# Performance work log

Hardware: AMD Instinct MI355X
Metric: run time of the kernel (lower is better)

Reference implementation:

```python
import jax, jax.numpy as jnp
import numpy as np
import math

B, S, D, H = 4, 1024, 1024, 16
DK = D // H
WINDOW = 128
NEG = -100000.0


def setup_inputs() -> dict:
    key = jax.random.key(0)
    kx, kw1, kb1, kw2, kb2 = jax.random.split(key, 5)
    x = jax.random.normal(kx, (B, S, D), dtype=jnp.float32)
    # sliding-window band mask: True where |i-j| <= WINDOW
    i = jnp.arange(S)
    band = (jnp.abs(i[:, None] - i[None, :]) <= WINDOW)
    mask = jnp.broadcast_to(band, (B, S, S))
    # second structured mask: causal
    causal = (i[:, None] >= i[None, :])
    mask2 = jnp.broadcast_to(causal, (B, S, S))
    scale = 1.0 / math.sqrt(D)
    Wqkv = jax.random.normal(kw1, (D, 3 * D), dtype=jnp.float32) * scale
    bqkv = jax.random.normal(kb1, (3 * D,), dtype=jnp.float32) * 0.01
    Wo = jax.random.normal(kw2, (D, D), dtype=jnp.float32) * scale
    bo = jax.random.normal(kb2, (D,), dtype=jnp.float32) * 0.01
    return {"x": x, "mask": mask, "mask2": mask2, "Wqkv": Wqkv, "bqkv": bqkv, "Wo": Wo, "bo": bo}


def reference(x, mask, mask2, Wqkv, bqkv, Wo, bo):
    b, s, d = x.shape
    qkv = x @ Wqkv + bqkv                      # [b, s, 3d]
    q, k, v = jnp.split(qkv, 3, axis=-1)
    # [b, s, h, dk] -> [b, h, s, dk]
    q = q.reshape(b, s, H, DK).transpose(0, 2, 1, 3)
    k = k.reshape(b, s, H, DK).transpose(0, 2, 1, 3)
    v = v.reshape(b, s, H, DK).transpose(0, 2, 1, 3)
    scores = jnp.einsum('bhtd,bhsd->bhts', q, k) / math.sqrt(DK)
    scores = jnp.where(mask[:, None, :, :], scores, NEG)
    scores = jnp.where(mask2[:, None, :, :], scores, NEG)
    weights = jax.nn.softmax(scores, axis=-1)  # [b, h, t, s]
    context = jnp.einsum('bhts,bhsd->bhtd', weights, v)
    context = context.transpose(0, 2, 1, 3).reshape(b, s, d)
    context = context @ Wo + bo
    return (context, weights)
```

## Files before the change

### kernel.cpp

```cpp
#include <hip/hip_runtime.h>

typedef short bf16x8 __attribute__((ext_vector_type(8)));
typedef float floatx4 __attribute__((ext_vector_type(4)));

#define GLOBAL_AS __attribute__((address_space(1)))
#define LDS_AS __attribute__((address_space(3)))

__device__ __forceinline__ void gload_lds16(const ushort* g, ushort* l) {
  __builtin_amdgcn_global_load_lds((const GLOBAL_AS void*)g, (LDS_AS void*)l, 16, 0, 0);
}

__device__ __forceinline__ ushort f2bf(float x) {
  uint u = __float_as_uint(x);
  return (ushort)((u + 0x7fffu + ((u >> 16) & 1u)) >> 16);
}

__global__ __launch_bounds__(256) void k_f32_to_bf16(const float4* __restrict__ in,
                                                     ushort4* __restrict__ out, int n4) {
  int g = blockIdx.x * 256 + threadIdx.x;
  if (g < n4) {
    float4 v = in[g];
    ushort4 o;
    o.x = f2bf(v.x); o.y = f2bf(v.y); o.z = f2bf(v.z); o.w = f2bf(v.w);
    out[g] = o;
  }
}

__global__ __launch_bounds__(256) void k_transpose2(const float* __restrict__ W1,
                                                    ushort* __restrict__ O1,
                                                    const float* __restrict__ W2,
                                                    ushort* __restrict__ O2) {
  __shared__ float tile[32][33];
  int bx = blockIdx.x;
  const float* in; ushort* out; int N;
  if (bx < 96) { in = W1; out = O1; N = 3072; }
  else         { in = W2; out = O2; N = 1024; bx -= 96; }
  const int K = 1024;
  int n0 = bx * 32, k0 = blockIdx.y * 32;
  int tx = threadIdx.x & 31, ty = threadIdx.x >> 5;
  #pragma unroll
  for (int r = ty; r < 32; r += 8)
    tile[r][tx] = in[(size_t)(k0 + r) * N + n0 + tx];
  __syncthreads();
  #pragma unroll
  for (int r = ty; r < 32; r += 8)
    out[(size_t)(n0 + r) * K + k0 + tx] = f2bf(tile[tx][r]);
}

template <int OUT_BF16, int BN>
__global__ __launch_bounds__(256) void k_gemm_bt(const ushort* __restrict__ A,
                                                 const ushort* __restrict__ Bt,
                                                 const float* __restrict__ bias,
                                                 void* __restrict__ Cout,
                                                 int M, int N, int K) {
  constexpr int NI = BN / 32;
  constexpr int NB = BN / 64;
  __shared__ ushort As[128 * 32];
  __shared__ ushort Bs[BN * 32];
  const int t = threadIdx.x;
  const int m0 = blockIdx.y * 128, n0 = blockIdx.x * BN;
  const int w = t >> 6, l = t & 63;
  const int wm = (w & 1) * 64, wn = (w >> 1) * (BN / 2);
  const int lr = l & 15, q8 = (l >> 4) * 8;
  const int lrow = l >> 2, lcol = (l & 3) * 8;

  floatx4 acc[4][NI];
  #pragma unroll
  for (int i = 0; i < 4; ++i)
    #pragma unroll
    for (int j = 0; j < NI; ++j) acc[i][j] = (floatx4){0.f, 0.f, 0.f, 0.f};

  for (int k0 = 0; k0 < K; k0 += 32) {
    __syncthreads();
    #pragma unroll
    for (int i = 0; i < 2; ++i) {
      int r0 = (w * 2 + i) * 16;
      gload_lds16(A + (size_t)(m0 + r0 + lrow) * K + k0 + lcol, As + r0 * 32);
    }
    #pragma unroll
    for (int i = 0; i < NB; ++i) {
      int r0 = (w * NB + i) * 16;
      gload_lds16(Bt + (size_t)(n0 + r0 + lrow) * K + k0 + lcol, Bs + r0 * 32);
    }
    __syncthreads();
    bf16x8 af[4], bfr[NI];
    #pragma unroll
    for (int mi = 0; mi < 4; ++mi)
      af[mi] = *(const bf16x8*)(As + (wm + mi * 16 + lr) * 32 + q8);
    #pragma unroll
    for (int ni = 0; ni < NI; ++ni)
      bfr[ni] = *(const bf16x8*)(Bs + (wn + ni * 16 + lr) * 32 + q8);
    #pragma unroll
    for (int mi = 0; mi < 4; ++mi)
      #pragma unroll
      for (int ni = 0; ni < NI; ++ni)
        acc[mi][ni] = __builtin_amdgcn_mfma_f32_16x16x32_bf16(af[mi], bfr[ni], acc[mi][ni], 0, 0, 0);
  }

  const int rq = (l >> 4) * 4;
  #pragma unroll
  for (int ni = 0; ni < NI; ++ni) {
    int col = n0 + wn + ni * 16 + lr;
    float bv = bias[col];
    #pragma unroll
    for (int mi = 0; mi < 4; ++mi) {
      int row = m0 + wm + mi * 16 + rq;
      #pragma unroll
      for (int r2 = 0; r2 < 4; ++r2) {
        float v = acc[mi][ni][r2] + bv;
        size_t idx = (size_t)(row + r2) * N + col;
        if (OUT_BF16) ((ushort*)Cout)[idx] = f2bf(v);
        else          ((float*)Cout)[idx] = v;
      }
    }
  }
}

__global__ __launch_bounds__(256) void k_attn(const ushort* __restrict__ qkv,
                                              float* __restrict__ wout,
                                              ushort* __restrict__ ctxout) {
  __shared__ float smA[64][68];
  __shared__ float smB[64 * 68];
  __shared__ float smInv[64];

  const int t = threadIdx.x;
  const int tj = t & 15, ti = t >> 4;
  const int iblk = blockIdx.x & 15;
  const int h = (blockIdx.x >> 4) & 15;
  const int b = blockIdx.x >> 8;
  const int i0 = iblk * 64;
  const int tok0 = b * 1024 + i0;
  const int qoff = h * 64, koff = 1024 + h * 64, voff = 2048 + h * 64;
  const size_t wbase = ((size_t)(b * 16 + h) * 1024 + i0) * 1024;

  {
    int jstart = i0 - 128; if (jstart < 0) jstart = 0;
    int jend = i0 + 64;
    float4 z = {0.f, 0.f, 0.f, 0.f};
    for (int g = t; g < 64 * 256; g += 256) {
      int r = g >> 8, j = (g & 255) * 4;
      if (j < jstart || j >= jend)
        *(float4*)(wout + wbase + (size_t)r * 1024 + j) = z;
    }
  }

  for (int cc = t; cc < 512; cc += 256) {
    int r = cc >> 3, c8 = (cc & 7) * 8;
    uint4 u = *(const uint4*)(qkv + (size_t)(tok0 + r) * 3072 + qoff + c8);
    float4 f0, f1;
    f0.x = __uint_as_float(u.x << 16); f0.y = __uint_as_float(u.x & 0xffff0000u);
    f0.z = __uint_as_float(u.y << 16); f0.w = __uint_as_float(u.y & 0xffff0000u);
    f1.x = __uint_as_float(u.z << 16); f1.y = __uint_as_float(u.z & 0xffff0000u);
    f1.z = __uint_as_float(u.w << 16); f1.w = __uint_as_float(u.w & 0xffff0000u);
    *(float4*)&smA[r][c8] = f0;
    *(float4*)&smA[r][c8 + 4] = f1;
  }

  float sreg[3][4][4];
  float mrun[4], lrun[4];
  #pragma unroll
  for (int ri = 0; ri < 4; ++ri) { mrun[ri] = -3e38f; lrun[ri] = 0.f; }

  #pragma unroll
  for (int bb = 0; bb < 3; ++bb) {
    const int jb = i0 - 128 + bb * 64;
    if (jb < 0) continue;
    __syncthreads();
    for (int cc = t; cc < 512; cc += 256) {
      int r = cc >> 3, c8 = (cc & 7) * 8;
      uint4 u = *(const uint4*)(qkv + (size_t)(b * 1024 + jb + r) * 3072 + koff + c8);
      float4 f0, f1;
      f0.x = __uint_as_float(u.x << 16); f0.y = __uint_as_float(u.x & 0xffff0000u);
      f0.z = __uint_as_float(u.y << 16); f0.w = __uint_as_float(u.y & 0xffff0000u);
      f1.x = __uint_as_float(u.z << 16); f1.y = __uint_as_float(u.z & 0xffff0000u);
      f1.z = __uint_as_float(u.w << 16); f1.w = __uint_as_float(u.w & 0xffff0000u);
      *(float4*)&smB[r * 68 + c8] = f0;
      *(float4*)&smB[r * 68 + c8 + 4] = f1;
    }
    __syncthreads();

    float sacc[4][4];
    #pragma unroll
    for (int ri = 0; ri < 4; ++ri)
      #pragma unroll
      for (int ci = 0; ci < 4; ++ci) sacc[ri][ci] = 0.f;

    for (int d4 = 0; d4 < 16; ++d4) {
      float4 qv[4], kv[4];
      #pragma unroll
      for (int ri = 0; ri < 4; ++ri) qv[ri] = *(const float4*)&smA[4 * ti + ri][d4 * 4];
      #pragma unroll
      for (int ci = 0; ci < 4; ++ci) kv[ci] = *(const float4*)&smB[(tj + 16 * ci) * 68 + d4 * 4];
      #pragma unroll
      for (int ri = 0; ri < 4; ++ri)
        #pragma unroll
        for (int ci = 0; ci < 4; ++ci)
          sacc[ri][ci] += qv[ri].x * kv[ci].x + qv[ri].y * kv[ci].y +
                          qv[ri].z * kv[ci].z + qv[ri].w * kv[ci].w;
    }

    #pragma unroll
    for (int ri = 0; ri < 4; ++ri) {
      int gi = i0 + 4 * ti + ri;
      float mx = mrun[ri];
      #pragma unroll
      for (int ci = 0; ci < 4; ++ci) {
        int gj = jb + tj + 16 * ci;
        bool valid = (gj <= gi) && (gi - gj <= 128);
        float s = valid ? sacc[ri][ci] * 0.125f : -3e38f;
        sreg[bb][ri][ci] = s;
        mx = fmaxf(mx, s);
      }
      float sum = lrun[ri] * __expf(mrun[ri] - mx);
      #pragma unroll
      for (int ci = 0; ci < 4; ++ci) {
        float s = sreg[bb][ri][ci];
        sum += (s > -1e37f) ? __expf(s - mx) : 0.f;
      }
      mrun[ri] = mx; lrun[ri] = sum;
    }
  }

  float mfin[4], minv[4];
  #pragma unroll
  for (int ri = 0; ri < 4; ++ri) {
    float m = mrun[ri], lsum = lrun[ri];
    #pragma unroll
    for (int off = 1; off < 16; off <<= 1) {
      float mo = __shfl_xor(m, off, 64);
      float lo = __shfl_xor(lsum, off, 64);
      float mn = fmaxf(m, mo);
      lsum = lsum * __expf(m - mn) + lo * __expf(mo - mn);
      m = mn;
    }
    mfin[ri] = m;
    minv[ri] = 1.0f / lsum;
  }
  if (tj == 0) {
    #pragma unroll
    for (int ri = 0; ri < 4; ++ri) smInv[4 * ti + ri] = minv[ri];
  }

  float ctx[4][4];
  #pragma unroll
  for (int ri = 0; ri < 4; ++ri)
    #pragma unroll
    for (int ci = 0; ci < 4; ++ci) ctx[ri][ci] = 0.f;

  #pragma unroll
  for (int bb = 0; bb < 3; ++bb) {
    const int jb = i0 - 128 + bb * 64;
    if (jb < 0) continue;
    __syncthreads();
    for (int cc = t; cc < 512; cc += 256) {
      int r = cc >> 3, c8 = (cc & 7) * 8;
      uint4 u = *(const uint4*)(qkv + (size_t)(b * 1024 + jb + r) * 3072 + voff + c8);
      float* bT = smB + r;
      bT[(c8 + 0) * 67] = __uint_as_float(u.x << 16);
      bT[(c8 + 1) * 67] = __uint_as_float(u.x & 0xffff0000u);
      bT[(c8 + 2) * 67] = __uint_as_float(u.y << 16);
      bT[(c8 + 3) * 67] = __uint_as_float(u.y & 0xffff0000u);
      bT[(c8 + 4) * 67] = __uint_as_float(u.z << 16);
      bT[(c8 + 5) * 67] = __uint_as_float(u.z & 0xffff0000u);
      bT[(c8 + 6) * 67] = __uint_as_float(u.w << 16);
      bT[(c8 + 7) * 67] = __uint_as_float(u.w & 0xffff0000u);
    }
    #pragma unroll
    for (int ri = 0; ri < 4; ++ri) {
      int r = 4 * ti + ri;
      float mr = mfin[ri];
      #pragma unroll
      for (int ci = 0; ci < 4; ++ci) {
        float s = sreg[bb][ri][ci];
        smA[r][tj + 16 * ci] = (s > -1e37f) ? __expf(s - mr) : 0.f;
      }
    }
    __syncthreads();
    for (int g = t; g < 1024; g += 256) {
      int r = g >> 4, c = (g & 15) * 4;
      float4 e4 = *(const float4*)&smA[r][c];
      float iv = smInv[r];
      float4 o = {e4.x * iv, e4.y * iv, e4.z * iv, e4.w * iv};
      *(float4*)(wout + wbase + (size_t)r * 1024 + jb + c) = o;
    }
    #pragma unroll 4
    for (int jl4 = 0; jl4 < 64; jl4 += 4) {
      float4 wv4[4], vv4[4];
      #pragma unroll
      for (int ri = 0; ri < 4; ++ri) wv4[ri] = *(const float4*)&smA[4 * ti + ri][jl4];
      #pragma unroll
      for (int ci = 0; ci < 4; ++ci) vv4[ci] = *(const float4*)(smB + (tj + 16 * ci) * 67 + jl4);
      #pragma unroll
      for (int ri = 0; ri < 4; ++ri)
        #pragma unroll
        for (int ci = 0; ci < 4; ++ci)
          ctx[ri][ci] += wv4[ri].x * vv4[ci].x + wv4[ri].y * vv4[ci].y +
                         wv4[ri].z * vv4[ci].z + wv4[ri].w * vv4[ci].w;
    }
  }

  #pragma unroll
  for (int ri = 0; ri < 4; ++ri) {
    int r = 4 * ti + ri;
    float iv = minv[ri];
    #pragma unroll
    for (int ci = 0; ci < 4; ++ci)
      ctxout[(size_t)(tok0 + r) * 1024 + qoff + tj + 16 * ci] = f2bf(ctx[ri][ci] * iv);
  }
}

extern "C" void kernel_launch(void* const* d_in, const int* in_sizes, int n_in,
                              void* d_out, int out_size, void* d_ws, size_t ws_size,
                              hipStream_t stream) {
  const float* x    = (const float*)d_in[0];
  const float* Wqkv = (const float*)d_in[3];
  const float* bqkv = (const float*)d_in[4];
  const float* Wo   = (const float*)d_in[5];
  const float* bo   = (const float*)d_in[6];

  float* out_ctx = (float*)d_out;
  float* out_w   = out_ctx + (size_t)4 * 1024 * 1024;

  char* ws = (char*)d_ws;
  ushort* qkv_bf = (ushort*)(ws);
  ushort* ctx_bf = (ushort*)(ws + 25165824);
  ushort* x_bf   = (ushort*)(ws + 33554432);
  ushort* WqkvT  = (ushort*)(ws + 41943040);
  ushort* WoT    = (ushort*)(ws + 48234496);

  k_f32_to_bf16<<<4096, 256, 0, stream>>>((const float4*)x, (ushort4*)x_bf, 1048576);
  k_transpose2<<<dim3(128, 32), 256, 0, stream>>>(Wqkv, WqkvT, Wo, WoT);
  k_gemm_bt<1, 128><<<dim3(24, 32), 256, 0, stream>>>(x_bf, WqkvT, bqkv, qkv_bf, 4096, 3072, 1024);
  k_attn<<<1024, 256, 0, stream>>>(qkv_bf, out_w, ctx_bf);
  k_gemm_bt<0, 64><<<dim3(16, 32), 256, 0, stream>>>(ctx_bf, WoT, bo, out_ctx, 4096, 1024, 1024);
}
```

Baseline: 443.6 us.

## Rewrite windowed attention kernel with bf16 MFMA and single-pass softmax

Replaces the scalar fp32 FMA attention kernel with one that uses bf16 MFMA 16x16x32 instructions for both QK^T and PV. All 192 K and V rows of the window are loaded into LDS at once, kept as bf16 (V stored transposed), so the three-block online softmax becomes a single pass with one max and one sum reduction. This removes the per-block syncs and the fp32 conversion work. In exchange it uses more LDS per block, writes the weights output as scattered scalar stores, and feeds bf16-rounded probabilities into PV.

```diff
diff --git a/kernel.cpp b/kernel.cpp
--- a/kernel.cpp
+++ b/kernel.cpp
@@ -119,22 +119,24 @@
 __global__ __launch_bounds__(256) void k_attn(const ushort* __restrict__ qkv,
                                               float* __restrict__ wout,
                                               ushort* __restrict__ ctxout) {
-  __shared__ float smA[64][68];
-  __shared__ float smB[64 * 68];
-  __shared__ float smInv[64];
+  __shared__ ushort smKP[192 * 68];
+  __shared__ ushort smVT[64 * 202];
+  __shared__ ushort smQ[64 * 68];
 
   const int t = threadIdx.x;
-  const int tj = t & 15, ti = t >> 4;
+  const int w = t >> 6, l = t & 63;
+  const int lr = l & 15, q8 = (l >> 4) * 8, q4 = (l >> 4) * 4;
   const int iblk = blockIdx.x & 15;
   const int h = (blockIdx.x >> 4) & 15;
   const int b = blockIdx.x >> 8;
   const int i0 = iblk * 64;
+  const int jb0 = i0 - 128;
   const int tok0 = b * 1024 + i0;
   const int qoff = h * 64, koff = 1024 + h * 64, voff = 2048 + h * 64;
   const size_t wbase = ((size_t)(b * 16 + h) * 1024 + i0) * 1024;
 
   {
-    int jstart = i0 - 128; if (jstart < 0) jstart = 0;
+    int jstart = jb0 < 0 ? 0 : jb0;
     int jend = i0 + 64;
     float4 z = {0.f, 0.f, 0.f, 0.f};
     for (int g = t; g < 64 * 256; g += 256) {
@@ -144,168 +146,125 @@
     }
   }
 
-  for (int cc = t; cc < 512; cc += 256) {
-    int r = cc >> 3, c8 = (cc & 7) * 8;
-    uint4 u = *(const uint4*)(qkv + (size_t)(tok0 + r) * 3072 + qoff + c8);
-    float4 f0, f1;
-    f0.x = __uint_as_float(u.x << 16); f0.y = __uint_as_float(u.x & 0xffff0000u);
-    f0.z = __uint_as_float(u.y << 16); f0.w = __uint_as_float(u.y & 0xffff0000u);
-    f1.x = __uint_as_float(u.z << 16); f1.y = __uint_as_float(u.z & 0xffff0000u);
-    f1.z = __uint_as_float(u.w << 16); f1.w = __uint_as_float(u.w & 0xffff0000u);
-    *(float4*)&smA[r][c8] = f0;
-    *(float4*)&smA[r][c8 + 4] = f1;
-  }
-
-  float sreg[3][4][4];
-  float mrun[4], lrun[4];
-  #pragma unroll
-  for (int ri = 0; ri < 4; ++ri) { mrun[ri] = -3e38f; lrun[ri] = 0.f; }
-
-  #pragma unroll
-  for (int bb = 0; bb < 3; ++bb) {
-    const int jb = i0 - 128 + bb * 64;
-    if (jb < 0) continue;
-    __syncthreads();
-    for (int cc = t; cc < 512; cc += 256) {
-      int r = cc >> 3, c8 = (cc & 7) * 8;
-      uint4 u = *(const uint4*)(qkv + (size_t)(b * 1024 + jb + r) * 3072 + koff + c8);
-      float4 f0, f1;
-      f0.x = __uint_as_float(u.x << 16); f0.y = __uint_as_float(u.x & 0xffff0000u);
-      f0.z = __uint_as_float(u.y << 16); f0.w = __uint_as_float(u.y & 0xffff0000u);
-      f1.x = __uint_as_float(u.z << 16); f1.y = __uint_as_float(u.z & 0xffff0000u);
-      f1.z = __uint_as_float(u.w << 16); f1.w = __uint_as_float(u.w & 0xffff0000u);
-      *(float4*)&smB[r * 68 + c8] = f0;
-      *(float4*)&smB[r * 68 + c8 + 4] = f1;
-    }
-    __syncthreads();
-
-    float sacc[4][4];
-    #pragma unroll
-    for (int ri = 0; ri < 4; ++ri)
-      #pragma unroll
-      for (int ci = 0; ci < 4; ++ci) sacc[ri][ci] = 0.f;
-
-    for (int d4 = 0; d4 < 16; ++d4) {
-      float4 qv[4], kv[4];
-      #pragma unroll
-      for (int ri = 0; ri < 4; ++ri) qv[ri] = *(const float4*)&smA[4 * ti + ri][d4 * 4];
-      #pragma unroll
-      for (int ci = 0; ci < 4; ++ci) kv[ci] = *(const float4*)&smB[(tj + 16 * ci) * 68 + d4 * 4];
-      #pragma unroll
-      for (int ri = 0; ri < 4; ++ri)
-        #pragma unroll
-        for (int ci = 0; ci < 4; ++ci)
-          sacc[ri][ci] += qv[ri].x * kv[ci].x + qv[ri].y * kv[ci].y +
-                          qv[ri].z * kv[ci].z + qv[ri].w * kv[ci].w;
-    }
-
-    #pragma unroll
-    for (int ri = 0; ri < 4; ++ri) {
-      int gi = i0 + 4 * ti + ri;
-      float mx = mrun[ri];
-      #pragma unroll
-      for (int ci = 0; ci < 4; ++ci) {
-        int gj = jb + tj + 16 * ci;
-        bool valid = (gj <= gi) && (gi - gj <= 128);
-        float s = valid ? sacc[ri][ci] * 0.125f : -3e38f;
-        sreg[bb][ri][ci] = s;
-        mx = fmaxf(mx, s);
-      }
-      float sum = lrun[ri] * __expf(mrun[ri] - mx);
-      #pragma unroll
-      for (int ci = 0; ci < 4; ++ci) {
-        float s = sreg[bb][ri][ci];
-        sum += (s > -1e37f) ? __expf(s - mx) : 0.f;
-      }
-      mrun[ri] = mx; lrun[ri] = sum;
-    }
-  }
-
-  float mfin[4], minv[4];
-  #pragma unroll
-  for (int ri = 0; ri < 4; ++ri) {
-    float m = mrun[ri], lsum = lrun[ri];
-    #pragma unroll
-    for (int off = 1; off < 16; off <<= 1) {
-      float mo = __shfl_xor(m, off, 64);
-      float lo = __shfl_xor(lsum, off, 64);
-      float mn = fmaxf(m, mo);
-      lsum = lsum * __expf(m - mn) + lo * __expf(mo - mn);
-      m = mn;
-    }
-    mfin[ri] = m;
-    minv[ri] = 1.0f / lsum;
-  }
-  if (tj == 0) {
-    #pragma unroll
-    for (int ri = 0; ri < 4; ++ri) smInv[4 * ti + ri] = minv[ri];
-  }
-
-  float ctx[4][4];
-  #pragma unroll
-  for (int ri = 0; ri < 4; ++ri)
-    #pragma unroll
-    for (int ci = 0; ci < 4; ++ci) ctx[ri][ci] = 0.f;
-
-  #pragma unroll
-  for (int bb = 0; bb < 3; ++bb) {
-    const int jb = i0 - 128 + bb * 64;
-    if (jb < 0) continue;
-    __syncthreads();
-    for (int cc = t; cc < 512; cc += 256) {
-      int r = cc >> 3, c8 = (cc & 7) * 8;
-      uint4 u = *(const uint4*)(qkv + (size_t)(b * 1024 + jb + r) * 3072 + voff + c8);
-      float* bT = smB + r;
-      bT[(c8 + 0) * 67] = __uint_as_float(u.x << 16);
-      bT[(c8 + 1) * 67] = __uint_as_float(u.x & 0xffff0000u);
-      bT[(c8 + 2) * 67] = __uint_as_float(u.y << 16);
-      bT[(c8 + 3) * 67] = __uint_as_float(u.y & 0xffff0000u);
-      bT[(c8 + 4) * 67] = __uint_as_float(u.z << 16);
-      bT[(c8 + 5) * 67] = __uint_as_float(u.z & 0xffff0000u);
-      bT[(c8 + 6) * 67] = __uint_as_float(u.w << 16);
-      bT[(c8 + 7) * 67] = __uint_as_float(u.w & 0xffff0000u);
-    }
-    #pragma unroll
-    for (int ri = 0; ri < 4; ++ri) {
-      int r = 4 * ti + ri;
-      float mr = mfin[ri];
-      #pragma unroll
-      for (int ci = 0; ci < 4; ++ci) {
-        float s = sreg[bb][ri][ci];
-        smA[r][tj + 16 * ci] = (s > -1e37f) ? __expf(s - mr) : 0.f;
-      }
-    }
-    __syncthreads();
-    for (int g = t; g < 1024; g += 256) {
-      int r = g >> 4, c = (g & 15) * 4;
-      float4 e4 = *(const float4*)&smA[r][c];
-      float iv = smInv[r];
-      float4 o = {e4.x * iv, e4.y * iv, e4.z * iv, e4.w * iv};
-      *(float4*)(wout + wbase + (size_t)r * 1024 + jb + c) = o;
-    }
-    #pragma unroll 4
-    for (int jl4 = 0; jl4 < 64; jl4 += 4) {
-      float4 wv4[4], vv4[4];
-      #pragma unroll
-      for (int ri = 0; ri < 4; ++ri) wv4[ri] = *(const float4*)&smA[4 * ti + ri][jl4];
-      #pragma unroll
-      for (int ci = 0; ci < 4; ++ci) vv4[ci] = *(const float4*)(smB + (tj + 16 * ci) * 67 + jl4);
-      #pragma unroll
-      for (int ri = 0; ri < 4; ++ri)
-        #pragma unroll
-        for (int ci = 0; ci < 4; ++ci)
-          ctx[ri][ci] += wv4[ri].x * vv4[ci].x + wv4[ri].y * vv4[ci].y +
-                         wv4[ri].z * vv4[ci].z + wv4[ri].w * vv4[ci].w;
-    }
-  }
-
-  #pragma unroll
-  for (int ri = 0; ri < 4; ++ri) {
-    int r = 4 * ti + ri;
-    float iv = minv[ri];
-    #pragma unroll
-    for (int ci = 0; ci < 4; ++ci)
-      ctxout[(size_t)(tok0 + r) * 1024 + qoff + tj + 16 * ci] = f2bf(ctx[ri][ci] * iv);
+  #pragma unroll
+  for (int c = 0; c < 2; ++c) {
+    int idx = t + 256 * c, row = idx >> 3, ch = idx & 7;
+    *(uint4*)(smQ + row * 68 + ch * 8) =
+        *(const uint4*)(qkv + (size_t)(tok0 + row) * 3072 + qoff + ch * 8);
+  }
+  #pragma unroll
+  for (int c = 0; c < 6; ++c) {
+    int idx = t + 256 * c, row = idx >> 3, ch = idx & 7;
+    int jsrc = jb0 + row; if (jsrc < 0) jsrc = 0;
+    *(uint4*)(smKP + row * 68 + ch * 8) =
+        *(const uint4*)(qkv + (size_t)(b * 1024 + jsrc) * 3072 + koff + ch * 8);
+  }
+  #pragma unroll
+  for (int c = 0; c < 6; ++c) {
+    int idx = t + 256 * c;
+    int j = (idx & 15) + 16 * (idx >> 7);
+    int d0 = ((idx >> 4) & 7) * 8;
+    int jsrc = jb0 + j; if (jsrc < 0) jsrc = 0;
+    uint4 u = *(const uint4*)(qkv + (size_t)(b * 1024 + jsrc) * 3072 + voff + d0);
+    ushort* p = smVT + j;
+    p[(d0 + 0) * 202] = (ushort)(u.x & 0xffffu);
+    p[(d0 + 1) * 202] = (ushort)(u.x >> 16);
+    p[(d0 + 2) * 202] = (ushort)(u.y & 0xffffu);
+    p[(d0 + 3) * 202] = (ushort)(u.y >> 16);
+    p[(d0 + 4) * 202] = (ushort)(u.z & 0xffffu);
+    p[(d0 + 5) * 202] = (ushort)(u.z >> 16);
+    p[(d0 + 6) * 202] = (ushort)(u.w & 0xffffu);
+    p[(d0 + 7) * 202] = (ushort)(u.w >> 16);
+  }
+  __syncthreads();
+
+  floatx4 sc[12];
+  #pragma unroll
+  for (int ni = 0; ni < 12; ++ni) sc[ni] = (floatx4){0.f, 0.f, 0.f, 0.f};
+  bf16x8 aq0 = *(const bf16x8*)(smQ + (w * 16 + lr) * 68 + q8);
+  bf16x8 aq1 = *(const bf16x8*)(smQ + (w * 16 + lr) * 68 + 32 + q8);
+  #pragma unroll
+  for (int ni = 0; ni < 12; ++ni) {
+    bf16x8 bk0 = *(const bf16x8*)(smKP + (ni * 16 + lr) * 68 + q8);
+    bf16x8 bk1 = *(const bf16x8*)(smKP + (ni * 16 + lr) * 68 + 32 + q8);
+    sc[ni] = __builtin_amdgcn_mfma_f32_16x16x32_bf16(aq0, bk0, sc[ni], 0, 0, 0);
+    sc[ni] = __builtin_amdgcn_mfma_f32_16x16x32_bf16(aq1, bk1, sc[ni], 0, 0, 0);
+  }
+  __syncthreads();
+
+  float mrow[4] = {-3e38f, -3e38f, -3e38f, -3e38f};
+  #pragma unroll
+  for (int ni = 0; ni < 12; ++ni) {
+    int nj = ni * 16 + lr;
+    #pragma unroll
+    for (int reg = 0; reg < 4; ++reg) {
+      int di = w * 16 + q4 + reg;
+      bool valid = (nj >= di) & (nj <= di + 128) & (jb0 + nj >= 0);
+      float s = valid ? sc[ni][reg] * 0.125f : -3e38f;
+      sc[ni][reg] = s;
+      mrow[reg] = fmaxf(mrow[reg], s);
+    }
+  }
+  #pragma unroll
+  for (int reg = 0; reg < 4; ++reg) {
+    #pragma unroll
+    for (int off = 1; off < 16; off <<= 1)
+      mrow[reg] = fmaxf(mrow[reg], __shfl_xor(mrow[reg], off, 64));
+  }
+  float lrow[4] = {0.f, 0.f, 0.f, 0.f};
+  #pragma unroll
+  for (int ni = 0; ni < 12; ++ni) {
+    #pragma unroll
+    for (int reg = 0; reg < 4; ++reg) {
+      float e = __expf(sc[ni][reg] - mrow[reg]);
+      sc[ni][reg] = e;
+      lrow[reg] += e;
+    }
+  }
+  float inv[4];
+  #pragma unroll
+  for (int reg = 0; reg < 4; ++reg) {
+    float s = lrow[reg];
+    #pragma unroll
+    for (int off = 1; off < 16; off <<= 1) s += __shfl_xor(s, off, 64);
+    inv[reg] = 1.0f / s;
+  }
+
+  ushort* smP = smKP;
+  #pragma unroll
+  for (int ni = 0; ni < 12; ++ni) {
+    int nj = ni * 16 + lr;
+    int j = jb0 + nj;
+    #pragma unroll
+    for (int reg = 0; reg < 4; ++reg) {
+      int il = w * 16 + q4 + reg;
+      float e = sc[ni][reg];
+      if (j >= 0) wout[wbase + (size_t)il * 1024 + j] = e * inv[reg];
+      smP[il * 202 + nj] = f2bf(e);
+    }
+  }
+
+  floatx4 oc[4];
+  #pragma unroll
+  for (int ni = 0; ni < 4; ++ni) oc[ni] = (floatx4){0.f, 0.f, 0.f, 0.f};
+  #pragma unroll
+  for (int ks = 0; ks < 6; ++ks) {
+    bf16x8 ap = *(const bf16x8*)(smP + (w * 16 + lr) * 202 + ks * 32 + q8);
+    #pragma unroll
+    for (int ni = 0; ni < 4; ++ni) {
+      bf16x8 bv = *(const bf16x8*)(smVT + (ni * 16 + lr) * 202 + ks * 32 + q8);
+      oc[ni] = __builtin_amdgcn_mfma_f32_16x16x32_bf16(ap, bv, oc[ni], 0, 0, 0);
+    }
+  }
+
+  #pragma unroll
+  for (int ni = 0; ni < 4; ++ni) {
+    int d = ni * 16 + lr;
+    #pragma unroll
+    for (int reg = 0; reg < 4; ++reg) {
+      int il = w * 16 + q4 + reg;
+      ctxout[(size_t)(tok0 + il) * 1024 + qoff + d] = f2bf(oc[ni][reg] * inv[reg]);
+    }
   }
 }
 
```

Measured after the change: 407.7 us. 8.1% less time.
